# Optimization experiments

Measured on AMD Instinct MI355X. Metric: run time of the kernel, lower is better.

## Reference

```python
import jax, jax.numpy as jnp
import numpy as np

T, B, OBS, H, GH = 512, 256, 512, 256, 256  # time, batch, obs_dim, FC_DIM_SIZE(=GRU hidden), GRU_HIDDEN_DIM (actor width)
ADIMS = (32, 32, 16, 64)
BIG = 1e10


def setup_inputs():
    key = jax.random.key(0)
    ks = jax.random.split(key, 16)
    f = lambda i, shp: (jax.random.normal(ks[i], shp, jnp.float32) / np.float32(np.sqrt(shp[0])))
    inp = {
        "hidden": jnp.zeros((B, H), jnp.float32),
        "obs": jax.random.normal(ks[0], (T, B, OBS), jnp.float32),
        "dones": jax.random.randint(ks[1], (T, B), 0, 2).astype(jnp.int32),
        "avail_lc1": jax.random.randint(ks[2], (T, B, ADIMS[0]), 0, 2).astype(jnp.int32),
        "avail_lc2": jax.random.randint(ks[3], (T, B, ADIMS[1]), 0, 2).astype(jnp.int32),
        "avail_mc": jax.random.randint(ks[4], (T, B, ADIMS[2]), 0, 2).astype(jnp.int32),
        "avail_hint": jax.random.randint(ks[5], (T, B, ADIMS[3]), 0, 2).astype(jnp.int32),
        "W_emb": f(6, (OBS, H)), "b_emb": jnp.zeros((H,), jnp.float32),
        "Wi": f(7, (H, 3 * H)), "bi": jnp.zeros((3 * H,), jnp.float32),
        "Wh": f(8, (H, 3 * H)), "bhn": jnp.zeros((H,), jnp.float32),
        "W_a": f(9, (H, GH)), "b_a": jnp.zeros((GH,), jnp.float32),
        "W_lc1": f(10, (GH, ADIMS[0])), "b_lc1": jnp.zeros((ADIMS[0],), jnp.float32),
        "W_lc2": f(11, (GH, ADIMS[1])), "b_lc2": jnp.zeros((ADIMS[1],), jnp.float32),
        "W_mc": f(12, (GH, ADIMS[2])), "b_mc": jnp.zeros((ADIMS[2],), jnp.float32),
        "W_hint": f(13, (GH, ADIMS[3])), "b_hint": jnp.zeros((ADIMS[3],), jnp.float32),
        "W_c1": f(14, (H, H)), "b_c1": jnp.zeros((H,), jnp.float32),
        "W_c2": f(15, (H, 1)), "b_c2": jnp.zeros((1,), jnp.float32),
    }
    return inp


def _gru_scan(hidden, emb, dones, Wi, bi, Wh, bhn):
    # flax GRUCell math: r=sig(ir+hr), z=sig(iz+hz), n=tanh(in + r*(hn+bhn)), h'=(1-z)*n + z*h
    def step(h, xt):
        e, d = xt  # e: [B,H], d: [B]
        h = jnp.where(d[:, None] != 0, jnp.zeros_like(h), h)  # per-step reset to zero carry
        gi = e @ Wi + bi   # [B,3H]
        gh = h @ Wh        # [B,3H]
        ir, iz, inn = jnp.split(gi, 3, axis=-1)
        hr, hz, hn = jnp.split(gh, 3, axis=-1)
        r = jax.nn.sigmoid(ir + hr)
        z = jax.nn.sigmoid(iz + hz)
        n = jnp.tanh(inn + r * (hn + bhn))
        nh = (1.0 - z) * n + z * h
        return nh, nh
    return jax.lax.scan(step, hidden, (emb, dones))


def reference(hidden, obs, dones, avail_lc1, avail_lc2, avail_mc, avail_hint,
              W_emb, b_emb, Wi, bi, Wh, bhn, W_a, b_a,
              W_lc1, b_lc1, W_lc2, b_lc2, W_mc, b_mc, W_hint, b_hint,
              W_c1, b_c1, W_c2, b_c2):
    emb = jax.nn.relu(obs @ W_emb + b_emb)                    # [T,B,H]
    hidden, y = _gru_scan(hidden, emb, dones, Wi, bi, Wh, bhn)  # y: [T,B,H]
    a = jax.nn.relu(y @ W_a + b_a)                            # [T,B,GH]
    mask = lambda logits, avail: logits - (1.0 - avail.astype(logits.dtype)) * BIG
    l_lc1 = mask(a @ W_lc1 + b_lc1, avail_lc1)
    l_lc2 = mask(a @ W_lc2 + b_lc2, avail_lc2)
    l_mc = mask(a @ W_mc + b_mc, avail_mc)
    l_hint = mask(a @ W_hint + b_hint, avail_hint)
    c = jax.nn.relu(y @ W_c1 + b_c1)                          # [T,B,H]
    critic = jnp.squeeze(c @ W_c2 + b_c2, axis=-1)            # [T,B]
    return (hidden, l_lc1, l_lc2, l_mc, l_hint, critic)
```

## Files before the change

### kernel.cpp

```cpp
#include <hip/hip_runtime.h>
#include <stdint.h>


typedef short short8 __attribute__((ext_vector_type(8)));
typedef float f32x4  __attribute__((ext_vector_type(4)));

#define T_DIM 512
#define CHUNK 32
#define NCH   16
#define GIPL  ((size_t)33554432)

#define OUT_HID  ((size_t)0)
#define OUT_LC1  ((size_t)65536)
#define OUT_LC2  ((size_t)4259840)
#define OUT_MC   ((size_t)8454144)
#define OUT_HINT ((size_t)10551296)
#define OUT_CRIT ((size_t)18939904)

__device__ __forceinline__ unsigned short f2bf(float f) {
    unsigned u = __float_as_uint(f);
    u += 0x7fffu + ((u >> 16) & 1u);
    return (unsigned short)(u >> 16);
}
__device__ __forceinline__ float bf2f(unsigned short h) {
    return __uint_as_float(((unsigned)h) << 16);
}

__device__ __forceinline__ unsigned short gru_cell(
    float ir, float iz, float inn, float ho,
    float hrv, float hzv, float hnv, float bh)
{
    float rg = 1.f / (1.f + __expf(-(ir + hrv)));
    float z  = 1.f / (1.f + __expf(-(iz + hzv)));
    float ex = __expf(2.f * (inn + rg * (hnv + bh)));
    float n  = 1.f - 2.f / (ex + 1.f);
    return f2bf((1.f - z) * n + z * ho);
}

__global__ __launch_bounds__(256, 4) void k_prep(
    const float* __restrict__ W_emb, const float* __restrict__ Wi,
    const float* __restrict__ Wh,    const float* __restrict__ W_a,
    const float* __restrict__ W_c1,  const float* __restrict__ W_lc1,
    const float* __restrict__ W_lc2, const float* __restrict__ W_mc,
    const float* __restrict__ W_hint,
    const float* __restrict__ b_lc1, const float* __restrict__ b_lc2,
    const float* __restrict__ b_mc,  const float* __restrict__ b_hint,
    unsigned short* __restrict__ WembT, unsigned short* __restrict__ WiT,
    unsigned short* __restrict__ WhF,   unsigned short* __restrict__ WacT,
    unsigned short* __restrict__ WlogT, float* __restrict__ blog,
    int* __restrict__ fixflag)
{
    int i = blockIdx.x * 256 + threadIdx.x;
    if (i < 131072) {
        int n = i >> 9, k = i & 511;
        WembT[i] = f2bf(W_emb[k * 256 + n]);
        return;
    }
    i -= 131072;
    if (i < 196608) {
        int n = i >> 8, k = i & 255;
        WiT[i] = f2bf(Wi[k * 768 + n]);
        return;
    }
    i -= 196608;
    if (i < 196608) {
        int jj = i & 7, L = (i >> 3) & 63, ks = (i >> 9) & 7, rest = i >> 12;
        int w = rest / 6, i6 = rest % 6, rho = i6 >> 1, s = i6 & 1;
        int k   = ks * 32 + ((L >> 4) << 3) + jj;
        int col = rho * 256 + w * 32 + s * 16 + (L & 15);
        WhF[i] = f2bf(Wh[k * 768 + col]);
        return;
    }
    i -= 196608;
    if (i < 131072) {
        int n = i >> 8, k = i & 255;
        WacT[i] = f2bf(n < 256 ? W_a[k * 256 + n] : W_c1[k * 256 + (n - 256)]);
        return;
    }
    i -= 131072;
    if (i < 40960) {
        int n = i >> 8, k = i & 255;
        float v;
        if      (n < 32)  v = W_lc1[k * 32 + n];
        else if (n < 64)  v = W_lc2[k * 32 + (n - 32)];
        else if (n < 80)  v = W_mc [k * 16 + (n - 64)];
        else if (n < 144) v = W_hint[k * 64 + (n - 80)];
        else              v = 0.f;
        WlogT[i] = f2bf(v);
        return;
    }
    i -= 40960;
    if (i < 160) {
        float v;
        if      (i < 32)  v = b_lc1[i];
        else if (i < 64)  v = b_lc2[i - 32];
        else if (i < 80)  v = b_mc [i - 64];
        else if (i < 144) v = b_hint[i - 80];
        else              v = 0.f;
        blog[i] = v;
        return;
    }
    i -= 160;
    if (i == 0) *fixflag = 0;
}

__global__ __launch_bounds__(512, 4) void k_fused_g12(
    const float* __restrict__ obs, const unsigned short* __restrict__ WembT,
    const float* __restrict__ b_emb, const unsigned short* __restrict__ WiT,
    const float* __restrict__ bi, unsigned short* __restrict__ out)
{
    __shared__ unsigned short As[64][72];
    __shared__ unsigned short Bs[256][72];
    __shared__ unsigned short eS[64][264];
    const int tid = threadIdx.x, w = tid >> 6, L = tid & 63;
    const int mq = (w >> 2) * 32, nq = (w & 3) * 64;
    const int m0 = blockIdx.x * 64;
    const int lc = L & 15, lq8 = (L >> 4) * 8, lr = (L >> 4) * 4;
    const int sra = tid >> 3, sha = (tid & 7) * 8;
    const int srb = tid >> 1, shb = (tid & 1) * 32;

    f32x4 acc[2][4];
#pragma unroll
    for (int i = 0; i < 2; i++)
#pragma unroll
        for (int j = 0; j < 4; j++) acc[i][j] = 0;

    const float* Ag = obs + (size_t)(m0 + sra) * 512 + sha;
    const unsigned short* Bg1 = WembT + (size_t)srb * 512 + shb;

    for (int kt = 0; kt < 512; kt += 64) {
        {
            f32x4 v0 = *(const f32x4*)(Ag + kt);
            f32x4 v1 = *(const f32x4*)(Ag + kt + 4);
            short8 pk;
            pk[0] = (short)f2bf(v0[0]); pk[1] = (short)f2bf(v0[1]);
            pk[2] = (short)f2bf(v0[2]); pk[3] = (short)f2bf(v0[3]);
            pk[4] = (short)f2bf(v1[0]); pk[5] = (short)f2bf(v1[1]);
            pk[6] = (short)f2bf(v1[2]); pk[7] = (short)f2bf(v1[3]);
            *(short8*)&As[sra][sha] = pk;
        }
#pragma unroll
        for (int c = 0; c < 32; c += 8)
            *(short8*)&Bs[srb][shb + c] = *(const short8*)(Bg1 + kt + c);
        __syncthreads();
#pragma unroll
        for (int ks = 0; ks < 2; ks++) {
            short8 a[2], b[4];
#pragma unroll
            for (int i = 0; i < 2; i++)
                a[i] = *(const short8*)&As[mq + i * 16 + lc][ks * 32 + lq8];
#pragma unroll
            for (int j = 0; j < 4; j++)
                b[j] = *(const short8*)&Bs[nq + j * 16 + lc][ks * 32 + lq8];
#pragma unroll
            for (int i = 0; i < 2; i++)
#pragma unroll
                for (int j = 0; j < 4; j++)
                    acc[i][j] = __builtin_amdgcn_mfma_f32_16x16x32_bf16(a[i], b[j], acc[i][j], 0, 0, 0);
        }
        __syncthreads();
    }
#pragma unroll
    for (int i = 0; i < 2; i++)
#pragma unroll
        for (int j = 0; j < 4; j++) {
            int col = nq + j * 16 + lc;
            float bv = b_emb[col];
#pragma unroll
            for (int rg = 0; rg < 4; rg++) {
                int row = mq + i * 16 + lr + rg;
                eS[row][col] = f2bf(fmaxf(acc[i][j][rg] + bv, 0.f));
            }
        }
    __syncthreads();

    for (int nc = 0; nc < 3; nc++) {
#pragma unroll
        for (int i = 0; i < 2; i++)
#pragma unroll
            for (int j = 0; j < 4; j++) acc[i][j] = 0;

        const unsigned short* Bg2 = WiT + (size_t)(nc * 256 + srb) * 256 + shb;
        for (int kt = 0; kt < 256; kt += 64) {
#pragma unroll
            for (int c = 0; c < 32; c += 8)
                *(short8*)&Bs[srb][shb + c] = *(const short8*)(Bg2 + kt + c);
            __syncthreads();
#pragma unroll
            for (int ks = 0; ks < 2; ks++) {
                short8 a[2], b[4];
#pragma unroll
                for (int i = 0; i < 2; i++)
                    a[i] = *(const short8*)&eS[mq + i * 16 + lc][kt + ks * 32 + lq8];
#pragma unroll
                for (int j = 0; j < 4; j++)
                    b[j] = *(const short8*)&Bs[nq + j * 16 + lc][ks * 32 + lq8];
#pragma unroll
                for (int i = 0; i < 2; i++)
#pragma unroll
                    for (int j = 0; j < 4; j++)
                        acc[i][j] = __builtin_amdgcn_mfma_f32_16x16x32_bf16(a[i], b[j], acc[i][j], 0, 0, 0);
            }
            __syncthreads();
        }
#pragma unroll
        for (int i = 0; i < 2; i++) {
            const int row0  = m0 + mq + i * 16 + lr;
            const int t     = row0 >> 8;
            const int g     = (row0 >> 4) & 15;
            const int rowg2 = (row0 >> 2) & 3;
#pragma unroll
            for (int jh = 0; jh < 2; jh++) {
                const int colb = nc * 256 + nq + jh * 32;
                const int gate = colb >> 8;
                const int w2   = (colb & 255) >> 5;
                short8 pk;
#pragma unroll
                for (int rg = 0; rg < 4; rg++)
#pragma unroll
                    for (int s = 0; s < 2; s++) {
                        int col = colb + s * 16 + lc;
                        float v = acc[i][jh * 2 + s][rg] + bi[col];
                        pk[rg * 2 + s] = (short)f2bf(v);
                    }
                size_t dst = (size_t)gate * GIPL +
                             (((size_t)(t * 16 + g) * 512) + (size_t)w2 * 64 +
                              (size_t)rowg2 * 16 + lc) * 8;
                *(short8*)(out + dst) = pk;
            }
        }
        __syncthreads();
    }
}

__global__ __launch_bounds__(512, 4) void k_gemm_ac(
    const unsigned short* __restrict__ y, const unsigned short* __restrict__ WacT,
    const float* __restrict__ b_a, const float* __restrict__ b_c1,
    unsigned short* __restrict__ out)
{
    __shared__ unsigned short yS[64][264];
    __shared__ unsigned short Bs[256][72];
    const int tid = threadIdx.x, w = tid >> 6, L = tid & 63;
    const int mq = (w >> 2) * 32, nq = (w & 3) * 64;
    const int m0 = blockIdx.x * 64;
    const int lc = L & 15, lq8 = (L >> 4) * 8, lr = (L >> 4) * 4;
    const int srb = tid >> 1, shb = (tid & 1) * 32;

    {
        int r = tid >> 3, cb = (tid & 7) * 32;
        const unsigned short* yg = y + (size_t)(m0 + r) * 256 + cb;
#pragma unroll
        for (int c = 0; c < 32; c += 8)
            *(short8*)&yS[r][cb + c] = *(const short8*)(yg + c);
    }

    f32x4 acc[2][4];
    for (int nc = 0; nc < 2; nc++) {
#pragma unroll
        for (int i = 0; i < 2; i++)
#pragma unroll
            for (int j = 0; j < 4; j++) acc[i][j] = 0;

        const unsigned short* Bg = WacT + (size_t)(nc * 256 + srb) * 256 + shb;
        for (int kt = 0; kt < 256; kt += 64) {
#pragma unroll
            for (int c = 0; c < 32; c += 8)
                *(short8*)&Bs[srb][shb + c] = *(const short8*)(Bg + kt + c);
            __syncthreads();
#pragma unroll
            for (int ks = 0; ks < 2; ks++) {
                short8 a[2], b[4];
#pragma unroll
                for (int i = 0; i < 2; i++)
                    a[i] = *(const short8*)&yS[mq + i * 16 + lc][kt + ks * 32 + lq8];
#pragma unroll
                for (int j = 0; j < 4; j++)
                    b[j] = *(const short8*)&Bs[nq + j * 16 + lc][ks * 32 + lq8];
#pragma unroll
                for (int i = 0; i < 2; i++)
#pragma unroll
                    for (int j = 0; j < 4; j++)
                        acc[i][j] = __builtin_amdgcn_mfma_f32_16x16x32_bf16(a[i], b[j], acc[i][j], 0, 0, 0);
            }
            __syncthreads();
        }
#pragma unroll
        for (int i = 0; i < 2; i++)
#pragma unroll
            for (int j = 0; j < 4; j++) {
                int col = nc * 256 + nq + j * 16 + lc;
                float bv = (col < 256) ? b_a[col] : b_c1[col - 256];
#pragma unroll
                for (int rg = 0; rg < 4; rg++) {
                    int row = m0 + mq + i * 16 + lr + rg;
                    out[(size_t)row * 512 + col] = f2bf(fmaxf(acc[i][j][rg] + bv, 0.f));
                }
            }
        __syncthreads();
    }
}

__global__ __launch_bounds__(512, 1) void k_gru_main(
    const unsigned short* __restrict__ gi, const unsigned short* __restrict__ WhF,
    const int* __restrict__ dones, const float* __restrict__ h0,
    const float* __restrict__ bhn, unsigned short* __restrict__ y,
    unsigned short* __restrict__ hend)
{
    __shared__ unsigned short hT[2][16][264];
    __shared__ unsigned short yS[2][16][256];
    __shared__ unsigned int rowbits[16];
    const int tid = threadIdx.x, w = tid >> 6, L = tid & 63;
    const int g = blockIdx.x & 15, c = blockIdx.x >> 4;
    const int b0 = g * 16, t0 = c * CHUNK;
    const int rowg = L >> 4, lc = L & 15;

    short8 Bf[6][8];
#pragma unroll
    for (int i6 = 0; i6 < 6; i6++)
#pragma unroll
        for (int ks = 0; ks < 8; ks++)
            Bf[i6][ks] = *(const short8*)(WhF + ((((size_t)w * 6 + i6) * 8 + ks) * 64 + L) * 8);

    const float bh0 = bhn[w * 32 + lc], bh1 = bhn[w * 32 + 16 + lc];

    if (tid < 16) rowbits[tid] = 0;
    __syncthreads();
    {
        int tp = tid >> 4, r = tid & 15;
        if (dones[(t0 + tp) * 256 + b0 + r]) atomicOr(&rowbits[r], 1u << tp);
    }
    __syncthreads();

    unsigned rbr[4];
#pragma unroll
    for (int r = 0; r < 4; r++) rbr[r] = rowbits[rowg * 4 + r];

    {
        int hrow = tid >> 5, hcol = (tid & 31) * 8;
        bool rz = (rowbits[hrow] & 1u) != 0;
#pragma unroll
        for (int cc = 0; cc < 8; cc++) {
            unsigned short v = 0;
            if (c == 0 && !rz) v = f2bf(h0[(b0 + hrow) * 256 + hcol + cc]);
            hT[0][hrow][hcol + cc] = v;
        }
    }
    __syncthreads();

    const size_t gstep = (size_t)16 * 512 * 8;
    size_t gb = ((size_t)(t0 * 16 + g) * 512 + tid) * 8;
    short8 vir = *(const short8*)(gi + gb);
    short8 viz = *(const short8*)(gi + GIPL + gb);
    short8 vin = *(const short8*)(gi + 2 * GIPL + gb);

#pragma unroll 2
    for (int tp = 0; tp < CHUNK; tp++) {
        const int cur = tp & 1, nxt = cur ^ 1;
        const int t = t0 + tp;

        short8 nir, niz, nin;
        if (tp + 1 < CHUNK) {
            size_t gn = gb + (size_t)(tp + 1) * gstep;
            nir = *(const short8*)(gi + gn);
            niz = *(const short8*)(gi + GIPL + gn);
            nin = *(const short8*)(gi + 2 * GIPL + gn);
        }

        f32x4 acc0 = 0, acc1 = 0, acc2 = 0, acc3 = 0, acc4 = 0, acc5 = 0;
#pragma unroll
        for (int ks = 0; ks < 8; ks++) {
            short8 a = *(const short8*)&hT[cur][lc][ks * 32 + rowg * 8];
            acc0 = __builtin_amdgcn_mfma_f32_16x16x32_bf16(a, Bf[0][ks], acc0, 0, 0, 0);
            acc1 = __builtin_amdgcn_mfma_f32_16x16x32_bf16(a, Bf[1][ks], acc1, 0, 0, 0);
            acc2 = __builtin_amdgcn_mfma_f32_16x16x32_bf16(a, Bf[2][ks], acc2, 0, 0, 0);
            acc3 = __builtin_amdgcn_mfma_f32_16x16x32_bf16(a, Bf[3][ks], acc3, 0, 0, 0);
            acc4 = __builtin_amdgcn_mfma_f32_16x16x32_bf16(a, Bf[4][ks], acc4, 0, 0, 0);
            acc5 = __builtin_amdgcn_mfma_f32_16x16x32_bf16(a, Bf[5][ks], acc5, 0, 0, 0);
        }

#pragma unroll
        for (int s = 0; s < 2; s++) {
            const int j = w * 32 + s * 16 + lc;
            f32x4 hrv = s ? acc1 : acc0;
            f32x4 hzv = s ? acc3 : acc2;
            f32x4 hnv = s ? acc5 : acc4;
            float bh = s ? bh1 : bh0;
#pragma unroll
            for (int r = 0; r < 4; r++) {
                int row = rowg * 4 + r;
                float ir  = bf2f((unsigned short)vir[r * 2 + s]);
                float iz  = bf2f((unsigned short)viz[r * 2 + s]);
                float inn = bf2f((unsigned short)vin[r * 2 + s]);
                float ho  = bf2f(hT[cur][row][j]);
                unsigned short hb = gru_cell(ir, iz, inn, ho, hrv[r], hzv[r], hnv[r], bh);
                yS[cur][row][j] = hb;
                unsigned short hw = hb;
                if (tp + 1 < CHUNK && ((rbr[r] >> (tp + 1)) & 1u)) hw = 0;
                hT[nxt][row][j] = hw;
            }
        }
        __syncthreads();

        {
            int yrow = tid >> 5, ycol = (tid & 31) * 8;
            short8 yv = *(const short8*)&yS[cur][yrow][ycol];
            *(short8*)(y + ((size_t)t * 256 + b0 + yrow) * 256 + ycol) = yv;
            if (tp == CHUNK - 1)
                *(short8*)(hend + ((size_t)c * 256 + b0 + yrow) * 256 + ycol) = yv;
        }

        vir = nir; viz = niz; vin = nin;
    }
}

__global__ __launch_bounds__(512, 1) void k_gru_fix_par(
    const unsigned short* __restrict__ gi, const unsigned short* __restrict__ WhF,
    const int* __restrict__ dones, const float* __restrict__ bhn,
    const unsigned short* __restrict__ hend, unsigned short* __restrict__ y,
    int* __restrict__ flag)
{
    __shared__ unsigned short hT[2][16][264];
    __shared__ unsigned int rowbits[16], prevbits[16];
    __shared__ int sh_fd[16];
    const int tid = threadIdx.x, w = tid >> 6, L = tid & 63;
    const int g = blockIdx.x & 15, c = (blockIdx.x >> 4) + 1;
    const int b0 = g * 16, t0 = c * CHUNK;
    const int rowg = L >> 4, lc = L & 15;
    const int hrow = tid >> 5, hcol = (tid & 31) * 8;

    short8 Bf[6][8];
#pragma unroll
    for (int i6 = 0; i6 < 6; i6++)
#pragma unroll
        for (int ks = 0; ks < 8; ks++)
            Bf[i6][ks] = *(const short8*)(WhF + ((((size_t)w * 6 + i6) * 8 + ks) * 64 + L) * 8);

    const float bh0 = bhn[w * 32 + lc], bh1 = bhn[w * 32 + 16 + lc];

    if (tid < 16) { rowbits[tid] = 0; prevbits[tid] = 0; }
    __syncthreads();
    {
        int tp = tid >> 4, r = tid & 15;
        if (dones[(t0 + tp) * 256 + b0 + r])         atomicOr(&rowbits[r],  1u << tp);
        if (dones[(t0 - CHUNK + tp) * 256 + b0 + r]) atomicOr(&prevbits[r], 1u << tp);
    }
    __syncthreads();
    if (tid < 16) {
        unsigned m = rowbits[tid];
        sh_fd[tid] = m ? __builtin_ctz(m) : CHUNK;
        if (prevbits[tid] == 0) atomicOr(flag, 1);
    }
    __syncthreads();

    int maxfix = 0;
    unsigned rbr[4]; int fdr[4];
#pragma unroll
    for (int r = 0; r < 16; r++) maxfix = max(maxfix, sh_fd[r]);
    if (maxfix == 0) return;
#pragma unroll
    for (int r = 0; r < 4; r++) {
        rbr[r] = rowbits[rowg * 4 + r];
        fdr[r] = sh_fd[rowg * 4 + r];
    }

    {
        short8 hv = *(const short8*)(hend + ((size_t)(c - 1) * 256 + b0 + hrow) * 256 + hcol);
        if (rowbits[hrow] & 1u) { short8 z = {0,0,0,0,0,0,0,0}; hv = z; }
        *(short8*)&hT[0][hrow][hcol] = hv;
    }
    __syncthreads();

    const size_t gstep = (size_t)16 * 512 * 8;
    const size_t gb0 = ((size_t)(t0 * 16 + g) * 512 + tid) * 8;

    int cur = 0;
    for (int tp = 0; tp < maxfix; tp++) {
        const int nxt = cur ^ 1;

        f32x4 acc0 = 0, acc1 = 0, acc2 = 0, acc3 = 0, acc4 = 0, acc5 = 0;
#pragma unroll
        for (int ks = 0; ks < 8; ks++) {
            short8 a = *(const short8*)&hT[cur][lc][ks * 32 + rowg * 8];
            acc0 = __builtin_amdgcn_mfma_f32_16x16x32_bf16(a, Bf[0][ks], acc0, 0, 0, 0);
            acc1 = __builtin_amdgcn_mfma_f32_16x16x32_bf16(a, Bf[1][ks], acc1, 0, 0, 0);
            acc2 = __builtin_amdgcn_mfma_f32_16x16x32_bf16(a, Bf[2][ks], acc2, 0, 0, 0);
            acc3 = __builtin_amdgcn_mfma_f32_16x16x32_bf16(a, Bf[3][ks], acc3, 0, 0, 0);
            acc4 = __builtin_amdgcn_mfma_f32_16x16x32_bf16(a, Bf[4][ks], acc4, 0, 0, 0);
            acc5 = __builtin_amdgcn_mfma_f32_16x16x32_bf16(a, Bf[5][ks], acc5, 0, 0, 0);
        }

        size_t gb = gb0 + (size_t)tp * gstep;
        short8 vir = *(const short8*)(gi + gb);
        short8 viz = *(const short8*)(gi + GIPL + gb);
        short8 vin = *(const short8*)(gi + 2 * GIPL + gb);

        unsigned short* yb = y + (size_t)((t0 + tp) * 256 + b0) * 256;
#pragma unroll
        for (int s = 0; s < 2; s++) {
            const int j = w * 32 + s * 16 + lc;
            f32x4 hrv = s ? acc1 : acc0;
            f32x4 hzv = s ? acc3 : acc2;
            f32x4 hnv = s ? acc5 : acc4;
            float bh = s ? bh1 : bh0;
#pragma unroll
            for (int r = 0; r < 4; r++) {
                int row = rowg * 4 + r;
                float ir  = bf2f((unsigned short)vir[r * 2 + s]);
                float iz  = bf2f((unsigned short)viz[r * 2 + s]);
                float inn = bf2f((unsigned short)vin[r * 2 + s]);
                float ho  = bf2f(hT[cur][row][j]);
                unsigned short hb = gru_cell(ir, iz, inn, ho, hrv[r], hzv[r], hnv[r], bh);
                if (tp < fdr[r]) yb[row * 256 + j] = hb;
                unsigned short hw = hb;
                if (tp + 1 < CHUNK && ((rbr[r] >> (tp + 1)) & 1u)) hw = 0;
                hT[nxt][row][j] = hw;
            }
        }
        __syncthreads();
        cur = nxt;
    }
}

__global__ __launch_bounds__(512, 1) void k_gru_fix(
    const unsigned short* __restrict__ gi, const unsigned short* __restrict__ WhF,
    const int* __restrict__ dones, const float* __restrict__ bhn,
    const unsigned short* __restrict__ hend, unsigned short* __restrict__ y,
    const int* __restrict__ flag)
{
    if (*flag == 0) return;

    __shared__ unsigned short hT[2][16][264];
    __shared__ unsigned int rowbits[16];
    __shared__ int sh_fd[16];
    const int tid = threadIdx.x, w = tid >> 6, L = tid & 63;
    const int b0 = blockIdx.x * 16, g = blockIdx.x;
    const int rowg = L >> 4, lc = L & 15;
    const int hrow = tid >> 5, hcol = (tid & 31) * 8;

    short8 Bf[6][8];
#pragma unroll
    for (int i6 = 0; i6 < 6; i6++)
#pragma unroll
        for (int ks = 0; ks < 8; ks++)
            Bf[i6][ks] = *(const short8*)(WhF + ((((size_t)w * 6 + i6) * 8 + ks) * 64 + L) * 8);

    const float bh0 = bhn[w * 32 + lc], bh1 = bhn[w * 32 + 16 + lc];

    *(short8*)&hT[0][hrow][hcol] =
        *(const short8*)(hend + (size_t)(b0 + hrow) * 256 + hcol);
    int cur = 0;

    const size_t gstep = (size_t)16 * 512 * 8;

    for (int c = 1; c < NCH; c++) {
        const int t0 = c * CHUNK;
        if (tid < 16) rowbits[tid] = 0;
        __syncthreads();
        {
            int tp = tid >> 4, r = tid & 15;
            if (dones[(t0 + tp) * 256 + b0 + r]) atomicOr(&rowbits[r], 1u << tp);
        }
        __syncthreads();
        if (tid < 16) {
            unsigned m = rowbits[tid];
            sh_fd[tid] = m ? __builtin_ctz(m) : CHUNK;
        }
        __syncthreads();

        int maxfix = 0;
        unsigned rbr[4]; int fdr[4];
#pragma unroll
        for (int r = 0; r < 16; r++) maxfix = max(maxfix, sh_fd[r]);
#pragma unroll
        for (int r = 0; r < 4; r++) {
            rbr[r] = rowbits[rowg * 4 + r];
            fdr[r] = sh_fd[rowg * 4 + r];
        }
        if (rowbits[hrow] & 1u) {
#pragma unroll
            for (int cc = 0; cc < 8; cc++) hT[cur][hrow][hcol + cc] = 0;
        }
        __syncthreads();

        const size_t gb0 = ((size_t)(t0 * 16 + g) * 512 + tid) * 8;

        for (int tp = 0; tp < maxfix; tp++) {
            const int nxt = cur ^ 1;

            f32x4 acc0 = 0, acc1 = 0, acc2 = 0, acc3 = 0, acc4 = 0, acc5 = 0;
#pragma unroll
            for (int ks = 0; ks < 8; ks++) {
                short8 a = *(const short8*)&hT[cur][lc][ks * 32 + rowg * 8];
                acc0 = __builtin_amdgcn_mfma_f32_16x16x32_bf16(a, Bf[0][ks], acc0, 0, 0, 0);
                acc1 = __builtin_amdgcn_mfma_f32_16x16x32_bf16(a, Bf[1][ks], acc1, 0, 0, 0);
                acc2 = __builtin_amdgcn_mfma_f32_16x16x32_bf16(a, Bf[2][ks], acc2, 0, 0, 0);
                acc3 = __builtin_amdgcn_mfma_f32_16x16x32_bf16(a, Bf[3][ks], acc3, 0, 0, 0);
                acc4 = __builtin_amdgcn_mfma_f32_16x16x32_bf16(a, Bf[4][ks], acc4, 0, 0, 0);
                acc5 = __builtin_amdgcn_mfma_f32_16x16x32_bf16(a, Bf[5][ks], acc5, 0, 0, 0);
            }

            size_t gb = gb0 + (size_t)tp * gstep;
            short8 vir = *(const short8*)(gi + gb);
            short8 viz = *(const short8*)(gi + GIPL + gb);
            short8 vin = *(const short8*)(gi + 2 * GIPL + gb);

            unsigned short* yb = y + (size_t)((t0 + tp) * 256 + b0) * 256;
#pragma unroll
            for (int s = 0; s < 2; s++) {
                const int j = w * 32 + s * 16 + lc;
                f32x4 hrv = s ? acc1 : acc0;
                f32x4 hzv = s ? acc3 : acc2;
                f32x4 hnv = s ? acc5 : acc4;
                float bh = s ? bh1 : bh0;
#pragma unroll
                for (int r = 0; r < 4; r++) {
                    int row = rowg * 4 + r;
                    float ir  = bf2f((unsigned short)vir[r * 2 + s]);
                    float iz  = bf2f((unsigned short)viz[r * 2 + s]);
                    float inn = bf2f((unsigned short)vin[r * 2 + s]);
                    float ho  = bf2f(hT[cur][row][j]);
                    unsigned short hb = gru_cell(ir, iz, inn, ho, hrv[r], hzv[r], hnv[r], bh);
                    if (tp < fdr[r]) yb[row * 256 + j] = hb;
                    unsigned short hw = hb;
                    if (tp + 1 < CHUNK && ((rbr[r] >> (tp + 1)) & 1u)) hw = 0;
                    hT[nxt][row][j] = hw;
                }
            }
            __syncthreads();
            cur = nxt;
        }

        if (sh_fd[hrow] < CHUNK) {
            *(short8*)&hT[cur][hrow][hcol] =
                *(const short8*)(hend + ((size_t)c * 256 + b0 + hrow) * 256 + hcol);
        }
        __syncthreads();
    }
}

__global__ __launch_bounds__(256, 2) void k_logits(
    const unsigned short* __restrict__ ac, const unsigned short* __restrict__ Bt,
    const float* __restrict__ blog,
    const int* __restrict__ av1, const int* __restrict__ av2,
    const int* __restrict__ av3, const int* __restrict__ av4,
    float* __restrict__ outp)
{
    __shared__ unsigned short As[128][72];
    __shared__ unsigned short Bs[160][72];
    const int tid = threadIdx.x, w = tid >> 6, L = tid & 63;
    const int m0 = blockIdx.x * 128;
    const int sr = tid >> 1, sh = (tid & 1) * 32;
    const int lc = L & 15, lq8 = (L >> 4) * 8, lr = (L >> 4) * 4;

    f32x4 acc[2][10];
#pragma unroll
    for (int i = 0; i < 2; i++)
#pragma unroll
        for (int j = 0; j < 10; j++) acc[i][j] = 0;

    const unsigned short* Ag = ac + (size_t)(m0 + sr) * 512 + sh;

    for (int kt = 0; kt < 256; kt += 64) {
#pragma unroll
        for (int c = 0; c < 32; c += 8)
            *(short8*)&As[sr][sh + c] = *(const short8*)(Ag + kt + c);
        for (int u = tid; u < 320; u += 256) {
            int br = u >> 1, bh2 = (u & 1) * 32;
#pragma unroll
            for (int c = 0; c < 32; c += 8)
                *(short8*)&Bs[br][bh2 + c] = *(const short8*)(Bt + (size_t)br * 256 + kt + bh2 + c);
        }
        __syncthreads();
#pragma unroll
        for (int ks = 0; ks < 2; ks++) {
            short8 a[2], b[10];
#pragma unroll
            for (int i = 0; i < 2; i++)
                a[i] = *(const short8*)&As[w * 32 + i * 16 + lc][ks * 32 + lq8];
#pragma unroll
            for (int j = 0; j < 10; j++)
                b[j] = *(const short8*)&Bs[j * 16 + lc][ks * 32 + lq8];
#pragma unroll
            for (int i = 0; i < 2; i++)
#pragma unroll
                for (int j = 0; j < 10; j++)
                    acc[i][j] = __builtin_amdgcn_mfma_f32_16x16x32_bf16(a[i], b[j], acc[i][j], 0, 0, 0);
        }
        __syncthreads();
    }
#pragma unroll
    for (int j = 0; j < 10; j++) {
        int col = j * 16 + lc;
        if (col >= 144) continue;
        int gbase, adim; const int* av; size_t obase;
        if      (col < 32) { gbase = 0;  adim = 32; av = av1; obase = OUT_LC1; }
        else if (col < 64) { gbase = 32; adim = 32; av = av2; obase = OUT_LC2; }
        else if (col < 80) { gbase = 64; adim = 16; av = av3; obase = OUT_MC;  }
        else               { gbase = 80; adim = 64; av = av4; obase = OUT_HINT;}
        int cof = col - gbase;
        float bv = blog[col];
#pragma unroll
        for (int i = 0; i < 2; i++)
#pragma unroll
            for (int rg = 0; rg < 4; rg++) {
                int R = m0 + w * 32 + i * 16 + lr + rg;
                float v = acc[i][j][rg] + bv;
                int a_ = av[(size_t)R * adim + cof];
                v -= (1.f - (float)a_) * 1e10f;
                outp[obase + (size_t)R * adim + cof] = v;
            }
    }
}

__global__ __launch_bounds__(256, 4) void k_critic(
    const unsigned short* __restrict__ ac, const float* __restrict__ W_c2,
    const float* __restrict__ b_c2, float* __restrict__ outp)
{
    const int tid = threadIdx.x, w = tid >> 6, L = tid & 63;
    f32x4 wv = *(const f32x4*)(W_c2 + L * 4);
    float bb = b_c2[0];
    int base = blockIdx.x * 64 + w * 16;
    for (int rr = 0; rr < 16; rr++) {
        int R = base + rr;
        const unsigned short* p = ac + (size_t)R * 512 + 256 + L * 4;
        float s = bf2f(p[0]) * wv[0] + bf2f(p[1]) * wv[1] +
                  bf2f(p[2]) * wv[2] + bf2f(p[3]) * wv[3];
#pragma unroll
        for (int o = 32; o > 0; o >>= 1) s += __shfl_down(s, o);
        if (L == 0) outp[OUT_CRIT + R] = s + bb;
    }
}

__global__ __launch_bounds__(256, 4) void k_hidden(
    const unsigned short* __restrict__ y, float* __restrict__ outp)
{
    int i = blockIdx.x * 256 + threadIdx.x;
    outp[OUT_HID + i] = bf2f(y[(size_t)511 * 65536 + i]);
}

extern "C" void kernel_launch(void* const* d_in, const int* in_sizes, int n_in,
                              void* d_out, int out_size, void* d_ws, size_t ws_size,
                              hipStream_t stream)
{
    const float* hidden = (const float*)d_in[0];
    const float* obs    = (const float*)d_in[1];
    const int*   dones  = (const int*)d_in[2];
    const int*   av1    = (const int*)d_in[3];
    const int*   av2    = (const int*)d_in[4];
    const int*   av3    = (const int*)d_in[5];
    const int*   av4    = (const int*)d_in[6];
    const float* W_emb  = (const float*)d_in[7];
    const float* b_emb  = (const float*)d_in[8];
    const float* Wi     = (const float*)d_in[9];
    const float* bi     = (const float*)d_in[10];
    const float* Wh     = (const float*)d_in[11];
    const float* bhn    = (const float*)d_in[12];
    const float* W_a    = (const float*)d_in[13];
    const float* b_a    = (const float*)d_in[14];
    const float* W_lc1  = (const float*)d_in[15];
    const float* b_lc1  = (const float*)d_in[16];
    const float* W_lc2  = (const float*)d_in[17];
    const float* b_lc2  = (const float*)d_in[18];
    const float* W_mc   = (const float*)d_in[19];
    const float* b_mc   = (const float*)d_in[20];
    const float* W_hint = (const float*)d_in[21];
    const float* b_hint = (const float*)d_in[22];
    const float* W_c1   = (const float*)d_in[23];
    const float* b_c1   = (const float*)d_in[24];
    const float* W_c2   = (const float*)d_in[25];
    const float* b_c2   = (const float*)d_in[26];

    char* ws = (char*)d_ws;
    unsigned short* WembT = (unsigned short*)(ws + 0);
    unsigned short* WiT   = (unsigned short*)(ws + 262144);
    unsigned short* WhF   = (unsigned short*)(ws + 655360);
    unsigned short* WacT  = (unsigned short*)(ws + 1048576);
    unsigned short* WlogT = (unsigned short*)(ws + 1310720);
    float*          blog  = (float*)(ws + 1392640);
    int*            fflag = (int*)(ws + 1393280);
    unsigned short* hend  = (unsigned short*)(ws + 1393664);
    unsigned short* ac    = hend;
    unsigned short* gibuf = (unsigned short*)(ws + 135611392);
    unsigned short* ybuf  = (unsigned short*)(ws + 336937984);
    float* outp = (float*)d_out;

    k_prep<<<2721, 256, 0, stream>>>(W_emb, Wi, Wh, W_a, W_c1, W_lc1, W_lc2,
                                     W_mc, W_hint, b_lc1, b_lc2, b_mc, b_hint,
                                     WembT, WiT, WhF, WacT, WlogT, blog, fflag);
    k_fused_g12<<<2048, 512, 0, stream>>>(obs, WembT, b_emb, WiT, bi, gibuf);
    k_gru_main<<<256, 512, 0, stream>>>(gibuf, WhF, dones, hidden, bhn, ybuf, hend);
    k_gru_fix_par<<<240, 512, 0, stream>>>(gibuf, WhF, dones, bhn, hend, ybuf, fflag);
    k_gru_fix<<<16, 512, 0, stream>>>(gibuf, WhF, dones, bhn, hend, ybuf, fflag);
    k_gemm_ac<<<2048, 512, 0, stream>>>(ybuf, WacT, b_a, b_c1, ac);
    k_logits<<<1024, 256, 0, stream>>>(ac, WlogT, blog, av1, av2, av3, av4, outp);
    k_critic<<<2048, 256, 0, stream>>>(ac, W_c2, b_c2, outp);
    k_hidden<<<2048 / 8, 256, 0, stream>>>(ybuf, outp);
}
```

Baseline: 922.4 us.

## Load GEMM MFMA operands directly from global memory, dropping LDS staging

The three parallel GEMM kernels (embedding+input gates, actor/critic hidden layer, logits) no longer stage A and B tiles through shared memory with __syncthreads. Each wave now loads its MFMA fragments straight from global memory in the MFMA lane layout, with partial unrolling. This removes LDS store/load traffic and barriers and frees shared memory, which may allow more blocks per CU. In exchange, operands shared between waves are fetched repeatedly from global memory and L2, and the loads are strided row fragments instead of coalesced tile loads. The GRU recurrence, which likely dominates the runtime, is unchanged.

```diff
diff --git a/kernel.cpp b/kernel.cpp
--- a/kernel.cpp
+++ b/kernel.cpp
@@ -109,15 +109,11 @@
     const float* __restrict__ b_emb, const unsigned short* __restrict__ WiT,
     const float* __restrict__ bi, unsigned short* __restrict__ out)
 {
-    __shared__ unsigned short As[64][72];
-    __shared__ unsigned short Bs[256][72];
     __shared__ unsigned short eS[64][264];
     const int tid = threadIdx.x, w = tid >> 6, L = tid & 63;
     const int mq = (w >> 2) * 32, nq = (w & 3) * 64;
     const int m0 = blockIdx.x * 64;
-    const int lc = L & 15, lq8 = (L >> 4) * 8, lr = (L >> 4) * 4;
-    const int sra = tid >> 3, sha = (tid & 7) * 8;
-    const int srb = tid >> 1, shb = (tid & 1) * 32;
+    const int lc = L & 15, g8 = (L >> 4) * 8, lr = (L >> 4) * 4;
 
     f32x4 acc[2][4];
 #pragma unroll
@@ -125,40 +121,39 @@
 #pragma unroll
         for (int j = 0; j < 4; j++) acc[i][j] = 0;
 
-    const float* Ag = obs + (size_t)(m0 + sra) * 512 + sha;
-    const unsigned short* Bg1 = WembT + (size_t)srb * 512 + shb;
-
-    for (int kt = 0; kt < 512; kt += 64) {
+    const float* a0p = obs + (size_t)(m0 + mq + lc) * 512 + g8;
+    const float* a1p = obs + (size_t)(m0 + mq + 16 + lc) * 512 + g8;
+#pragma unroll 4
+    for (int kk = 0; kk < 512; kk += 32) {
+        short8 a[2], b[4];
         {
-            f32x4 v0 = *(const f32x4*)(Ag + kt);
-            f32x4 v1 = *(const f32x4*)(Ag + kt + 4);
+            f32x4 v0 = *(const f32x4*)(a0p + kk);
+            f32x4 v1 = *(const f32x4*)(a0p + kk + 4);
             short8 pk;
             pk[0] = (short)f2bf(v0[0]); pk[1] = (short)f2bf(v0[1]);
             pk[2] = (short)f2bf(v0[2]); pk[3] = (short)f2bf(v0[3]);
             pk[4] = (short)f2bf(v1[0]); pk[5] = (short)f2bf(v1[1]);
             pk[6] = (short)f2bf(v1[2]); pk[7] = (short)f2bf(v1[3]);
-            *(short8*)&As[sra][sha] = pk;
-        }
-#pragma unroll
-        for (int c = 0; c < 32; c += 8)
-            *(short8*)&Bs[srb][shb + c] = *(const short8*)(Bg1 + kt + c);
-        __syncthreads();
-#pragma unroll
-        for (int ks = 0; ks < 2; ks++) {
-            short8 a[2], b[4];
-#pragma unroll
-            for (int i = 0; i < 2; i++)
-                a[i] = *(const short8*)&As[mq + i * 16 + lc][ks * 32 + lq8];
+            a[0] = pk;
+        }
+        {
+            f32x4 v0 = *(const f32x4*)(a1p + kk);
+            f32x4 v1 = *(const f32x4*)(a1p + kk + 4);
+            short8 pk;
+            pk[0] = (short)f2bf(v0[0]); pk[1] = (short)f2bf(v0[1]);
+            pk[2] = (short)f2bf(v0[2]); pk[3] = (short)f2bf(v0[3]);
+            pk[4] = (short)f2bf(v1[0]); pk[5] = (short)f2bf(v1[1]);
+            pk[6] = (short)f2bf(v1[2]); pk[7] = (short)f2bf(v1[3]);
+            a[1] = pk;
+        }
+#pragma unroll
+        for (int j = 0; j < 4; j++)
+            b[j] = *(const short8*)(WembT + (size_t)(nq + j * 16 + lc) * 512 + kk + g8);
+#pragma unroll
+        for (int i = 0; i < 2; i++)
 #pragma unroll
             for (int j = 0; j < 4; j++)
-                b[j] = *(const short8*)&Bs[nq + j * 16 + lc][ks * 32 + lq8];
-#pragma unroll
-            for (int i = 0; i < 2; i++)
-#pragma unroll
-                for (int j = 0; j < 4; j++)
-                    acc[i][j] = __builtin_amdgcn_mfma_f32_16x16x32_bf16(a[i], b[j], acc[i][j], 0, 0, 0);
-        }
-        __syncthreads();
+                acc[i][j] = __builtin_amdgcn_mfma_f32_16x16x32_bf16(a[i], b[j], acc[i][j], 0, 0, 0);
     }
 #pragma unroll
     for (int i = 0; i < 2; i++)
@@ -180,28 +175,20 @@
 #pragma unroll
             for (int j = 0; j < 4; j++) acc[i][j] = 0;
 
-        const unsigned short* Bg2 = WiT + (size_t)(nc * 256 + srb) * 256 + shb;
-        for (int kt = 0; kt < 256; kt += 64) {
-#pragma unroll
-            for (int c = 0; c < 32; c += 8)
-                *(short8*)&Bs[srb][shb + c] = *(const short8*)(Bg2 + kt + c);
-            __syncthreads();
-#pragma unroll
-            for (int ks = 0; ks < 2; ks++) {
-                short8 a[2], b[4];
-#pragma unroll
-                for (int i = 0; i < 2; i++)
-                    a[i] = *(const short8*)&eS[mq + i * 16 + lc][kt + ks * 32 + lq8];
+#pragma unroll 2
+        for (int kk = 0; kk < 256; kk += 32) {
+            short8 a[2], b[4];
+#pragma unroll
+            for (int i = 0; i < 2; i++)
+                a[i] = *(const short8*)&eS[mq + i * 16 + lc][kk + g8];
+#pragma unroll
+            for (int j = 0; j < 4; j++)
+                b[j] = *(const short8*)(WiT + (size_t)(nc * 256 + nq + j * 16 + lc) * 256 + kk + g8);
+#pragma unroll
+            for (int i = 0; i < 2; i++)
 #pragma unroll
                 for (int j = 0; j < 4; j++)
-                    b[j] = *(const short8*)&Bs[nq + j * 16 + lc][ks * 32 + lq8];
-#pragma unroll
-                for (int i = 0; i < 2; i++)
-#pragma unroll
-                    for (int j = 0; j < 4; j++)
-                        acc[i][j] = __builtin_amdgcn_mfma_f32_16x16x32_bf16(a[i], b[j], acc[i][j], 0, 0, 0);
-            }
-            __syncthreads();
+                    acc[i][j] = __builtin_amdgcn_mfma_f32_16x16x32_bf16(a[i], b[j], acc[i][j], 0, 0, 0);
         }
 #pragma unroll
         for (int i = 0; i < 2; i++) {
@@ -229,7 +216,6 @@
                 *(short8*)(out + dst) = pk;
             }
         }
-        __syncthreads();
     }
 }
 
@@ -238,51 +224,34 @@
     const float* __restrict__ b_a, const float* __restrict__ b_c1,
     unsigned short* __restrict__ out)
 {
-    __shared__ unsigned short yS[64][264];
-    __shared__ unsigned short Bs[256][72];
     const int tid = threadIdx.x, w = tid >> 6, L = tid & 63;
     const int mq = (w >> 2) * 32, nq = (w & 3) * 64;
     const int m0 = blockIdx.x * 64;
-    const int lc = L & 15, lq8 = (L >> 4) * 8, lr = (L >> 4) * 4;
-    const int srb = tid >> 1, shb = (tid & 1) * 32;
-
-    {
-        int r = tid >> 3, cb = (tid & 7) * 32;
-        const unsigned short* yg = y + (size_t)(m0 + r) * 256 + cb;
-#pragma unroll
-        for (int c = 0; c < 32; c += 8)
-            *(short8*)&yS[r][cb + c] = *(const short8*)(yg + c);
-    }
-
-    f32x4 acc[2][4];
+    const int lc = L & 15, g8 = (L >> 4) * 8, lr = (L >> 4) * 4;
+
+    const unsigned short* a0p = y + (size_t)(m0 + mq + lc) * 256 + g8;
+    const unsigned short* a1p = y + (size_t)(m0 + mq + 16 + lc) * 256 + g8;
+
     for (int nc = 0; nc < 2; nc++) {
+        f32x4 acc[2][4];
 #pragma unroll
         for (int i = 0; i < 2; i++)
 #pragma unroll
             for (int j = 0; j < 4; j++) acc[i][j] = 0;
 
-        const unsigned short* Bg = WacT + (size_t)(nc * 256 + srb) * 256 + shb;
-        for (int kt = 0; kt < 256; kt += 64) {
-#pragma unroll
-            for (int c = 0; c < 32; c += 8)
-                *(short8*)&Bs[srb][shb + c] = *(const short8*)(Bg + kt + c);
-            __syncthreads();
-#pragma unroll
-            for (int ks = 0; ks < 2; ks++) {
-                short8 a[2], b[4];
-#pragma unroll
-                for (int i = 0; i < 2; i++)
-                    a[i] = *(const short8*)&yS[mq + i * 16 + lc][kt + ks * 32 + lq8];
+#pragma unroll 2
+        for (int kk = 0; kk < 256; kk += 32) {
+            short8 a[2], b[4];
+            a[0] = *(const short8*)(a0p + kk);
+            a[1] = *(const short8*)(a1p + kk);
+#pragma unroll
+            for (int j = 0; j < 4; j++)
+                b[j] = *(const short8*)(WacT + (size_t)(nc * 256 + nq + j * 16 + lc) * 256 + kk + g8);
+#pragma unroll
+            for (int i = 0; i < 2; i++)
 #pragma unroll
                 for (int j = 0; j < 4; j++)
-                    b[j] = *(const short8*)&Bs[nq + j * 16 + lc][ks * 32 + lq8];
-#pragma unroll
-                for (int i = 0; i < 2; i++)
-#pragma unroll
-                    for (int j = 0; j < 4; j++)
-                        acc[i][j] = __builtin_amdgcn_mfma_f32_16x16x32_bf16(a[i], b[j], acc[i][j], 0, 0, 0);
-            }
-            __syncthreads();
+                    acc[i][j] = __builtin_amdgcn_mfma_f32_16x16x32_bf16(a[i], b[j], acc[i][j], 0, 0, 0);
         }
 #pragma unroll
         for (int i = 0; i < 2; i++)
@@ -296,7 +265,6 @@
                     out[(size_t)row * 512 + col] = f2bf(fmaxf(acc[i][j][rg] + bv, 0.f));
                 }
             }
-        __syncthreads();
     }
 }
 
@@ -645,12 +613,9 @@
     const int* __restrict__ av3, const int* __restrict__ av4,
     float* __restrict__ outp)
 {
-    __shared__ unsigned short As[128][72];
-    __shared__ unsigned short Bs[160][72];
     const int tid = threadIdx.x, w = tid >> 6, L = tid & 63;
     const int m0 = blockIdx.x * 128;
-    const int sr = tid >> 1, sh = (tid & 1) * 32;
-    const int lc = L & 15, lq8 = (L >> 4) * 8, lr = (L >> 4) * 4;
+    const int lc = L & 15, g8 = (L >> 4) * 8, lr = (L >> 4) * 4;
 
     f32x4 acc[2][10];
 #pragma unroll
@@ -658,35 +623,22 @@
 #pragma unroll
         for (int j = 0; j < 10; j++) acc[i][j] = 0;
 
-    const unsigned short* Ag = ac + (size_t)(m0 + sr) * 512 + sh;
-
-    for (int kt = 0; kt < 256; kt += 64) {
-#pragma unroll
-        for (int c = 0; c < 32; c += 8)
-            *(short8*)&As[sr][sh + c] = *(const short8*)(Ag + kt + c);
-        for (int u = tid; u < 320; u += 256) {
-            int br = u >> 1, bh2 = (u & 1) * 32;
-#pragma unroll
-            for (int c = 0; c < 32; c += 8)
-                *(short8*)&Bs[br][bh2 + c] = *(const short8*)(Bt + (size_t)br * 256 + kt + bh2 + c);
-        }
-        __syncthreads();
-#pragma unroll
-        for (int ks = 0; ks < 2; ks++) {
-            short8 a[2], b[10];
-#pragma unroll
-            for (int i = 0; i < 2; i++)
-                a[i] = *(const short8*)&As[w * 32 + i * 16 + lc][ks * 32 + lq8];
+    const unsigned short* a0p = ac + (size_t)(m0 + w * 32 + lc) * 512 + g8;
+    const unsigned short* a1p = ac + (size_t)(m0 + w * 32 + 16 + lc) * 512 + g8;
+
+#pragma unroll 2
+    for (int kk = 0; kk < 256; kk += 32) {
+        short8 a[2], b[10];
+        a[0] = *(const short8*)(a0p + kk);
+        a[1] = *(const short8*)(a1p + kk);
+#pragma unroll
+        for (int j = 0; j < 10; j++)
+            b[j] = *(const short8*)(Bt + (size_t)(j * 16 + lc) * 256 + kk + g8);
+#pragma unroll
+        for (int i = 0; i < 2; i++)
 #pragma unroll
             for (int j = 0; j < 10; j++)
-                b[j] = *(const short8*)&Bs[j * 16 + lc][ks * 32 + lq8];
-#pragma unroll
-            for (int i = 0; i < 2; i++)
-#pragma unroll
-                for (int j = 0; j < 10; j++)
-                    acc[i][j] = __builtin_amdgcn_mfma_f32_16x16x32_bf16(a[i], b[j], acc[i][j], 0, 0, 0);
-        }
-        __syncthreads();
+                acc[i][j] = __builtin_amdgcn_mfma_f32_16x16x32_bf16(a[i], b[j], acc[i][j], 0, 0, 0);
     }
 #pragma unroll
     for (int j = 0; j < 10; j++) {
```

New measurement: 1.252 ms. 35.8% more time.

## Pre-swizzle weights into MFMA fragment layout and load B operands directly from global

Applied to the files above, without the earlier changes.

The prep kernel now writes the embedding, input-gate, actor/critic and logit weights in a per-lane MFMA fragment order, so each wave can load its B operands straight from global memory (served from L2) with one contiguous 16-byte load per lane. The shared-memory B tiles, their staging copies and most block barriers in the three GEMM kernels are removed, cutting LDS traffic and synchronisation. The cost is that every wave re-reads weights from the cache hierarchy instead of sharing them through LDS, which may raise L2 pressure and load latency. Launch bounds drop from 4 to 3 blocks per SM.

```diff
diff --git a/kernel.cpp b/kernel.cpp
--- a/kernel.cpp
+++ b/kernel.cpp
@@ -45,21 +45,27 @@
     const float* __restrict__ W_hint,
     const float* __restrict__ b_lc1, const float* __restrict__ b_lc2,
     const float* __restrict__ b_mc,  const float* __restrict__ b_hint,
-    unsigned short* __restrict__ WembT, unsigned short* __restrict__ WiT,
-    unsigned short* __restrict__ WhF,   unsigned short* __restrict__ WacT,
-    unsigned short* __restrict__ WlogT, float* __restrict__ blog,
+    unsigned short* __restrict__ WembF, unsigned short* __restrict__ WiF,
+    unsigned short* __restrict__ WhF,   unsigned short* __restrict__ WacF,
+    unsigned short* __restrict__ WlogF, float* __restrict__ blog,
     int* __restrict__ fixflag)
 {
     int i = blockIdx.x * 256 + threadIdx.x;
     if (i < 131072) {
-        int n = i >> 9, k = i & 511;
-        WembT[i] = f2bf(W_emb[k * 256 + n]);
+        int jj = i & 7, L = (i >> 3) & 63, kt32 = (i >> 9) & 15;
+        int j = (i >> 13) & 3, q = (i >> 15) & 3;
+        int n = q * 64 + j * 16 + (L & 15);
+        int k = kt32 * 32 + ((L >> 4) << 3) + jj;
+        WembF[i] = f2bf(W_emb[k * 256 + n]);
         return;
     }
     i -= 131072;
     if (i < 196608) {
-        int n = i >> 8, k = i & 255;
-        WiT[i] = f2bf(Wi[k * 768 + n]);
+        int jj = i & 7, L = (i >> 3) & 63, kk32 = (i >> 9) & 7;
+        int j = (i >> 12) & 3, q = (i >> 14) & 3, nc = i >> 16;
+        int n = nc * 256 + q * 64 + j * 16 + (L & 15);
+        int k = kk32 * 32 + ((L >> 4) << 3) + jj;
+        WiF[i] = f2bf(Wi[k * 768 + n]);
         return;
     }
     i -= 196608;
@@ -73,20 +79,26 @@
     }
     i -= 196608;
     if (i < 131072) {
-        int n = i >> 8, k = i & 255;
-        WacT[i] = f2bf(n < 256 ? W_a[k * 256 + n] : W_c1[k * 256 + (n - 256)]);
+        int jj = i & 7, L = (i >> 3) & 63, kk32 = (i >> 9) & 7;
+        int j = (i >> 12) & 3, q = (i >> 14) & 3, nc = (i >> 16) & 1;
+        int n = nc * 256 + q * 64 + j * 16 + (L & 15);
+        int k = kk32 * 32 + ((L >> 4) << 3) + jj;
+        WacF[i] = f2bf(n < 256 ? W_a[k * 256 + n] : W_c1[k * 256 + (n - 256)]);
         return;
     }
     i -= 131072;
     if (i < 40960) {
-        int n = i >> 8, k = i & 255;
+        int jj = i & 7, L = (i >> 3) & 63, kk32 = (i >> 9) & 7;
+        int j = i >> 12;
+        int n = j * 16 + (L & 15);
+        int k = kk32 * 32 + ((L >> 4) << 3) + jj;
         float v;
         if      (n < 32)  v = W_lc1[k * 32 + n];
         else if (n < 64)  v = W_lc2[k * 32 + (n - 32)];
         else if (n < 80)  v = W_mc [k * 16 + (n - 64)];
         else if (n < 144) v = W_hint[k * 64 + (n - 80)];
         else              v = 0.f;
-        WlogT[i] = f2bf(v);
+        WlogF[i] = f2bf(v);
         return;
     }
     i -= 40960;
@@ -104,20 +116,18 @@
     if (i == 0) *fixflag = 0;
 }
 
-__global__ __launch_bounds__(512, 4) void k_fused_g12(
-    const float* __restrict__ obs, const unsigned short* __restrict__ WembT,
-    const float* __restrict__ b_emb, const unsigned short* __restrict__ WiT,
+__global__ __launch_bounds__(512, 3) void k_fused_g12(
+    const float* __restrict__ obs, const unsigned short* __restrict__ WembF,
+    const float* __restrict__ b_emb, const unsigned short* __restrict__ WiF,
     const float* __restrict__ bi, unsigned short* __restrict__ out)
 {
     __shared__ unsigned short As[64][72];
-    __shared__ unsigned short Bs[256][72];
     __shared__ unsigned short eS[64][264];
     const int tid = threadIdx.x, w = tid >> 6, L = tid & 63;
-    const int mq = (w >> 2) * 32, nq = (w & 3) * 64;
+    const int mq = (w >> 2) * 32, wq = w & 3, nq = wq * 64;
     const int m0 = blockIdx.x * 64;
     const int lc = L & 15, lq8 = (L >> 4) * 8, lr = (L >> 4) * 4;
     const int sra = tid >> 3, sha = (tid & 7) * 8;
-    const int srb = tid >> 1, shb = (tid & 1) * 32;
 
     f32x4 acc[2][4];
 #pragma unroll
@@ -126,8 +136,6 @@
         for (int j = 0; j < 4; j++) acc[i][j] = 0;
 
     const float* Ag = obs + (size_t)(m0 + sra) * 512 + sha;
-    const unsigned short* Bg1 = WembT + (size_t)srb * 512 + shb;
-
     for (int kt = 0; kt < 512; kt += 64) {
         {
             f32x4 v0 = *(const f32x4*)(Ag + kt);
@@ -139,19 +147,18 @@
             pk[6] = (short)f2bf(v1[2]); pk[7] = (short)f2bf(v1[3]);
             *(short8*)&As[sra][sha] = pk;
         }
-#pragma unroll
-        for (int c = 0; c < 32; c += 8)
-            *(short8*)&Bs[srb][shb + c] = *(const short8*)(Bg1 + kt + c);
         __syncthreads();
 #pragma unroll
         for (int ks = 0; ks < 2; ks++) {
+            const int kt32 = (kt >> 5) + ks;
             short8 a[2], b[4];
 #pragma unroll
             for (int i = 0; i < 2; i++)
                 a[i] = *(const short8*)&As[mq + i * 16 + lc][ks * 32 + lq8];
 #pragma unroll
             for (int j = 0; j < 4; j++)
-                b[j] = *(const short8*)&Bs[nq + j * 16 + lc][ks * 32 + lq8];
+                b[j] = *(const short8*)(WembF +
+                        ((((size_t)(wq * 4 + j) * 16 + kt32) * 64 + L) * 8));
 #pragma unroll
             for (int i = 0; i < 2; i++)
 #pragma unroll
@@ -180,28 +187,22 @@
 #pragma unroll
             for (int j = 0; j < 4; j++) acc[i][j] = 0;
 
-        const unsigned short* Bg2 = WiT + (size_t)(nc * 256 + srb) * 256 + shb;
-        for (int kt = 0; kt < 256; kt += 64) {
-#pragma unroll
-            for (int c = 0; c < 32; c += 8)
-                *(short8*)&Bs[srb][shb + c] = *(const short8*)(Bg2 + kt + c);
-            __syncthreads();
-#pragma unroll
-            for (int ks = 0; ks < 2; ks++) {
-                short8 a[2], b[4];
-#pragma unroll
-                for (int i = 0; i < 2; i++)
-                    a[i] = *(const short8*)&eS[mq + i * 16 + lc][kt + ks * 32 + lq8];
+#pragma unroll 2
+        for (int kk = 0; kk < 256; kk += 32) {
+            const int kk32 = kk >> 5;
+            short8 a[2], b[4];
+#pragma unroll
+            for (int i = 0; i < 2; i++)
+                a[i] = *(const short8*)&eS[mq + i * 16 + lc][kk + lq8];
+#pragma unroll
+            for (int j = 0; j < 4; j++)
+                b[j] = *(const short8*)(WiF +
+                        ((((size_t)((nc * 4 + wq) * 4 + j) * 8 + kk32) * 64 + L) * 8));
+#pragma unroll
+            for (int i = 0; i < 2; i++)
 #pragma unroll
                 for (int j = 0; j < 4; j++)
-                    b[j] = *(const short8*)&Bs[nq + j * 16 + lc][ks * 32 + lq8];
-#pragma unroll
-                for (int i = 0; i < 2; i++)
-#pragma unroll
-                    for (int j = 0; j < 4; j++)
-                        acc[i][j] = __builtin_amdgcn_mfma_f32_16x16x32_bf16(a[i], b[j], acc[i][j], 0, 0, 0);
-            }
-            __syncthreads();
+                    acc[i][j] = __builtin_amdgcn_mfma_f32_16x16x32_bf16(a[i], b[j], acc[i][j], 0, 0, 0);
         }
 #pragma unroll
         for (int i = 0; i < 2; i++) {
@@ -229,22 +230,19 @@
                 *(short8*)(out + dst) = pk;
             }
         }
-        __syncthreads();
-    }
-}
-
-__global__ __launch_bounds__(512, 4) void k_gemm_ac(
-    const unsigned short* __restrict__ y, const unsigned short* __restrict__ WacT,
+    }
+}
+
+__global__ __launch_bounds__(512, 3) void k_gemm_ac(
+    const unsigned short* __restrict__ y, const unsigned short* __restrict__ WacF,
     const float* __restrict__ b_a, const float* __restrict__ b_c1,
     unsigned short* __restrict__ out)
 {
     __shared__ unsigned short yS[64][264];
-    __shared__ unsigned short Bs[256][72];
     const int tid = threadIdx.x, w = tid >> 6, L = tid & 63;
-    const int mq = (w >> 2) * 32, nq = (w & 3) * 64;
+    const int mq = (w >> 2) * 32, wq = w & 3, nq = wq * 64;
     const int m0 = blockIdx.x * 64;
     const int lc = L & 15, lq8 = (L >> 4) * 8, lr = (L >> 4) * 4;
-    const int srb = tid >> 1, shb = (tid & 1) * 32;
 
     {
         int r = tid >> 3, cb = (tid & 7) * 32;
@@ -253,36 +251,31 @@
         for (int c = 0; c < 32; c += 8)
             *(short8*)&yS[r][cb + c] = *(const short8*)(yg + c);
     }
-
-    f32x4 acc[2][4];
+    __syncthreads();
+
     for (int nc = 0; nc < 2; nc++) {
+        f32x4 acc[2][4];
 #pragma unroll
         for (int i = 0; i < 2; i++)
 #pragma unroll
             for (int j = 0; j < 4; j++) acc[i][j] = 0;
 
-        const unsigned short* Bg = WacT + (size_t)(nc * 256 + srb) * 256 + shb;
-        for (int kt = 0; kt < 256; kt += 64) {
-#pragma unroll
-            for (int c = 0; c < 32; c += 8)
-                *(short8*)&Bs[srb][shb + c] = *(const short8*)(Bg + kt + c);
-            __syncthreads();
-#pragma unroll
-            for (int ks = 0; ks < 2; ks++) {
-                short8 a[2], b[4];
-#pragma unroll
-                for (int i = 0; i < 2; i++)
-                    a[i] = *(const short8*)&yS[mq + i * 16 + lc][kt + ks * 32 + lq8];
+#pragma unroll 2
+        for (int kk = 0; kk < 256; kk += 32) {
+            const int kk32 = kk >> 5;
+            short8 a[2], b[4];
+#pragma unroll
+            for (int i = 0; i < 2; i++)
+                a[i] = *(const short8*)&yS[mq + i * 16 + lc][kk + lq8];
+#pragma unroll
+            for (int j = 0; j < 4; j++)
+                b[j] = *(const short8*)(WacF +
+                        ((((size_t)((nc * 4 + wq) * 4 + j) * 8 + kk32) * 64 + L) * 8));
+#pragma unroll
+            for (int i = 0; i < 2; i++)
 #pragma unroll
                 for (int j = 0; j < 4; j++)
-                    b[j] = *(const short8*)&Bs[nq + j * 16 + lc][ks * 32 + lq8];
-#pragma unroll
-                for (int i = 0; i < 2; i++)
-#pragma unroll
-                    for (int j = 0; j < 4; j++)
-                        acc[i][j] = __builtin_amdgcn_mfma_f32_16x16x32_bf16(a[i], b[j], acc[i][j], 0, 0, 0);
-            }
-            __syncthreads();
+                    acc[i][j] = __builtin_amdgcn_mfma_f32_16x16x32_bf16(a[i], b[j], acc[i][j], 0, 0, 0);
         }
 #pragma unroll
         for (int i = 0; i < 2; i++)
@@ -296,7 +289,6 @@
                     out[(size_t)row * 512 + col] = f2bf(fmaxf(acc[i][j][rg] + bv, 0.f));
                 }
             }
-        __syncthreads();
     }
 }
 
@@ -639,14 +631,13 @@
 }
 
 __global__ __launch_bounds__(256, 2) void k_logits(
-    const unsigned short* __restrict__ ac, const unsigned short* __restrict__ Bt,
+    const unsigned short* __restrict__ ac, const unsigned short* __restrict__ WlogF,
     const float* __restrict__ blog,
     const int* __restrict__ av1, const int* __restrict__ av2,
     const int* __restrict__ av3, const int* __restrict__ av4,
     float* __restrict__ outp)
 {
     __shared__ unsigned short As[128][72];
-    __shared__ unsigned short Bs[160][72];
     const int tid = threadIdx.x, w = tid >> 6, L = tid & 63;
     const int m0 = blockIdx.x * 128;
     const int sr = tid >> 1, sh = (tid & 1) * 32;
@@ -664,22 +655,17 @@
 #pragma unroll
         for (int c = 0; c < 32; c += 8)
             *(short8*)&As[sr][sh + c] = *(const short8*)(Ag + kt + c);
-        for (int u = tid; u < 320; u += 256) {
-            int br = u >> 1, bh2 = (u & 1) * 32;
-#pragma unroll
-            for (int c = 0; c < 32; c += 8)
-                *(short8*)&Bs[br][bh2 + c] = *(const short8*)(Bt + (size_t)br * 256 + kt + bh2 + c);
-        }
         __syncthreads();
 #pragma unroll
         for (int ks = 0; ks < 2; ks++) {
+            const int kk32 = (kt >> 5) + ks;
             short8 a[2], b[10];
 #pragma unroll
             for (int i = 0; i < 2; i++)
                 a[i] = *(const short8*)&As[w * 32 + i * 16 + lc][ks * 32 + lq8];
 #pragma unroll
             for (int j = 0; j < 10; j++)
-                b[j] = *(const short8*)&Bs[j * 16 + lc][ks * 32 + lq8];
+                b[j] = *(const short8*)(WlogF + ((((size_t)j * 8 + kk32) * 64 + L) * 8));
 #pragma unroll
             for (int i = 0; i < 2; i++)
 #pragma unroll
@@ -771,11 +757,11 @@
     const float* b_c2   = (const float*)d_in[26];
 
     char* ws = (char*)d_ws;
-    unsigned short* WembT = (unsigned short*)(ws + 0);
-    unsigned short* WiT   = (unsigned short*)(ws + 262144);
+    unsigned short* WembF = (unsigned short*)(ws + 0);
+    unsigned short* WiF   = (unsigned short*)(ws + 262144);
     unsigned short* WhF   = (unsigned short*)(ws + 655360);
-    unsigned short* WacT  = (unsigned short*)(ws + 1048576);
-    unsigned short* WlogT = (unsigned short*)(ws + 1310720);
+    unsigned short* WacF  = (unsigned short*)(ws + 1048576);
+    unsigned short* WlogF = (unsigned short*)(ws + 1310720);
     float*          blog  = (float*)(ws + 1392640);
     int*            fflag = (int*)(ws + 1393280);
     unsigned short* hend  = (unsigned short*)(ws + 1393664);
@@ -786,13 +772,13 @@
 
     k_prep<<<2721, 256, 0, stream>>>(W_emb, Wi, Wh, W_a, W_c1, W_lc1, W_lc2,
                                      W_mc, W_hint, b_lc1, b_lc2, b_mc, b_hint,
-                                     WembT, WiT, WhF, WacT, WlogT, blog, fflag);
-    k_fused_g12<<<2048, 512, 0, stream>>>(obs, WembT, b_emb, WiT, bi, gibuf);
+                                     WembF, WiF, WhF, WacF, WlogF, blog, fflag);
+    k_fused_g12<<<2048, 512, 0, stream>>>(obs, WembF, b_emb, WiF, bi, gibuf);
     k_gru_main<<<256, 512, 0, stream>>>(gibuf, WhF, dones, hidden, bhn, ybuf, hend);
     k_gru_fix_par<<<240, 512, 0, stream>>>(gibuf, WhF, dones, bhn, hend, ybuf, fflag);
     k_gru_fix<<<16, 512, 0, stream>>>(gibuf, WhF, dones, bhn, hend, ybuf, fflag);
-    k_gemm_ac<<<2048, 512, 0, stream>>>(ybuf, WacT, b_a, b_c1, ac);
-    k_logits<<<1024, 256, 0, stream>>>(ac, WlogT, blog, av1, av2, av3, av4, outp);
+    k_gemm_ac<<<2048, 512, 0, stream>>>(ybuf, WacF, b_a, b_c1, ac);
+    k_logits<<<1024, 256, 0, stream>>>(ac, WlogF, blog, av1, av2, av3, av4, outp);
     k_critic<<<2048, 256, 0, stream>>>(ac, W_c2, b_c2, outp);
     k_hidden<<<2048 / 8, 256, 0, stream>>>(ybuf, outp);
 }
```

Measured after the change: 873.6 us. 1.06x faster.
